# Kernel optimization log

Measured on AMD Instinct MI355X. Metric: run time of the kernel, lower is better.

Reference implementation:

```python
import jax, jax.numpy as jnp
import numpy as np

# FP4 lookup table (E2M1-style values) exactly as in FP4Codec.FP4_TABLE
FP4_TABLE = jnp.array([0.0, 0.5, 1.0, 1.5, 2.0, 3.0, 4.0, 6.0,
                       0.0, -0.5, -1.0, -1.5, -2.0, -3.0, -4.0, -6.0],
                      dtype=jnp.float32)

M, K, N = 128, 4096, 16384


def setup_inputs() -> dict:
    key = jax.random.key(0)
    k1, k2, k3, k4 = jax.random.split(key, 4)
    x = jax.random.normal(k1, (M, K), dtype=jnp.float32)
    # packed bytes: each int holds two 4-bit FP4 indices (hi<<4 | lo)
    weight_fp4 = jax.random.randint(k2, (N, K // 2), 0, 256, dtype=jnp.int32)
    # positive per-output-channel scale (encode guarantees >= 1e-8)
    weight_scale = jax.random.uniform(k3, (N,), dtype=jnp.float32,
                                      minval=1e-3, maxval=2e-2)
    bias = jax.random.normal(k4, (N,), dtype=jnp.float32) * 0.02
    return {"x": x, "weight_fp4": weight_fp4,
            "weight_scale": weight_scale, "bias": bias}


def _dequantize(weight_fp4, weight_scale):
    p = weight_fp4.astype(jnp.uint8)
    hi = (p >> 4) & 0xF
    lo = p & 0xF
    # interleave [hi, lo] along last dim -> [N, K] indices
    idx = jnp.stack([hi, lo], axis=-1).reshape(p.shape[0], -1)
    return FP4_TABLE[idx] * weight_scale[:, None]  # [N, K] fp32


def reference(x, weight_fp4, weight_scale, bias):
    w = _dequantize(weight_fp4, weight_scale)          # [N, K]
    y = jnp.einsum('mk,nk->mn', x, w) + bias            # [M, N]
    return jax.nn.gelu(y, approximate=False)            # exact GELU like F.gelu
```

## Files before the change

kernel.cpp:

```cpp
#include <hip/hip_runtime.h>
#include <stdint.h>


#define M_DIM 128
#define K_DIM 4096
#define N_DIM 16384
#define BN    64
#define BK    64
#define NK    (K_DIM/BK)
#define NT    512
#define NBLK  (N_DIM/BN)

#define A_BYTES 16384
#define B_BYTES 8192
#define NBUF    4
#define AOFF(b) ((b)*A_BYTES)
#define BOFF(b) (NBUF*A_BYTES + (b)*B_BYTES)
#define LDS_SZ  (NBUF*(A_BYTES+B_BYTES))

typedef __attribute__((ext_vector_type(8))) __bf16 bf16x8;
typedef __attribute__((ext_vector_type(4))) float  f32x4;
typedef unsigned short ushort_t;

__device__ __forceinline__ unsigned f2b_bits(float f) {
  unsigned u = __builtin_bit_cast(unsigned, f);
  u += 0x7FFFu + ((u >> 16) & 1u);
  return u >> 16;
}

__global__ __launch_bounds__(256) void convert_x_kernel(
    const float* __restrict__ x, ushort_t* __restrict__ xb) {
  int i = (blockIdx.x * blockDim.x + threadIdx.x) * 4;
  float4 v = *(const float4*)(x + i);
  ushort4 p;
  p.x = (ushort_t)f2b_bits(v.x);
  p.y = (ushort_t)f2b_bits(v.y);
  p.z = (ushort_t)f2b_bits(v.z);
  p.w = (ushort_t)f2b_bits(v.w);
  *(ushort4*)(xb + i) = p;
}

__device__ __forceinline__ void gl16(const void* g, void* l) {
  __builtin_amdgcn_global_load_lds(
      (const __attribute__((address_space(1))) void*)g,
      (__attribute__((address_space(3))) void*)l, 16, 0, 0);
}

__device__ __forceinline__ bf16x8 decode8(uint4 p) {
  unsigned u01 = __builtin_amdgcn_perm(p.y, p.x, 0x04000400u);
  unsigned u23 = __builtin_amdgcn_perm(p.w, p.z, 0x04000400u);
  unsigned q   = __builtin_amdgcn_perm(u23, u01, 0x05040100u);
  unsigned e  = (q >> 4) & 0x0F0F0F0Fu;
  unsigned o  = q & 0x0F0F0F0Fu;
  unsigned em = e & 0x07070707u, om = o & 0x07070707u;
  unsigned elo = __builtin_amdgcn_perm(0xC0804000u, 0xC0800000u, em);
  unsigned ehi = __builtin_amdgcn_perm(0x40404040u, 0x3F3F3F00u, em);
  unsigned olo = __builtin_amdgcn_perm(0xC0804000u, 0xC0800000u, om);
  unsigned ohi = __builtin_amdgcn_perm(0x40404040u, 0x3F3F3F00u, om);
  ehi |= (e & 0x08080808u) << 4;
  ohi |= (o & 0x08080808u) << 4;
  unsigned t0 = __builtin_amdgcn_perm(ehi, elo, 0x05010400u);
  unsigned t1 = __builtin_amdgcn_perm(ohi, olo, 0x05010400u);
  unsigned t2 = __builtin_amdgcn_perm(ehi, elo, 0x07030602u);
  unsigned t3 = __builtin_amdgcn_perm(ohi, olo, 0x07030602u);
  uint4 r;
  r.x = __builtin_amdgcn_perm(t1, t0, 0x05040100u);
  r.y = __builtin_amdgcn_perm(t1, t0, 0x07060302u);
  r.z = __builtin_amdgcn_perm(t3, t2, 0x05040100u);
  r.w = __builtin_amdgcn_perm(t3, t2, 0x07060302u);
  return __builtin_bit_cast(bf16x8, r);
}

#define MFMA16(a_, b_, c_) __builtin_amdgcn_mfma_f32_16x16x32_bf16(a_, b_, c_, 0, 0, 0)

template<bool USE_XB>
__global__ __launch_bounds__(NT) void fp4gemm_kernel(
    const void* __restrict__ xsrc,
    const int*  __restrict__ wq,
    const float* __restrict__ scale,
    const float* __restrict__ bias,
    float* __restrict__ out) {
  __shared__ __align__(16) uint8_t lds[LDS_SZ];

  const int t   = threadIdx.x;
  const int w   = t >> 6;
  const int l   = t & 63;
  const int l16 = l & 15;
  const int lq  = l >> 4;
  const int kh  = w >> 2;
  const int mh  = (w >> 1) & 1;
  const int nh  = w & 1;

  const int bid = blockIdx.x;
  const int n0  = ((bid & 7) * (NBLK / 8) + (bid >> 3)) * BN;

  const int srow = t >> 3;
  const int scol = (t & 7) * 16;
  const int sswz = (srow & 7) << 4;
  const int scbs = scol ^ sswz;
  const int bwr  = srow * 128 + (scol ^ sswz);

  const uint8_t* xb  = (const uint8_t*)xsrc;
  const uint8_t* wqb = (const uint8_t*)wq;

  uint4 rq0, rq1, rq2, rq3;

#define ISSUE_A(k_, b_) do { \
  gl16(xb + (size_t)(srow) * 8192 + (size_t)(k_) * 128 + scbs, \
       lds + AOFF(b_) + w * 1024); \
  gl16(xb + (size_t)(64 + srow) * 8192 + (size_t)(k_) * 128 + scbs, \
       lds + AOFF(b_) + 8192 + w * 1024); \
} while (0)

#define ISSUE_B(k_, s_) do { \
  rq##s_ = *(const uint4*)(wqb + (size_t)(n0 + srow) * 8192 + \
                           (size_t)(k_) * 128 + scol); \
} while (0)

#define DECODE_B(s_, b_) do { \
  *(bf16x8*)(lds + BOFF(b_) + bwr) = decode8(rq##s_); \
} while (0)

#define WAITV(N_) asm volatile("s_waitcnt vmcnt(" #N_ ")" ::: "memory")
#define BARRIER() do { \
  asm volatile("s_waitcnt lgkmcnt(0)" ::: "memory"); \
  __builtin_amdgcn_s_barrier(); \
  __builtin_amdgcn_sched_barrier(0); \
} while (0)

  f32x4 acc[4][2] = {{{0,0,0,0},{0,0,0,0}},{{0,0,0,0},{0,0,0,0}},
                     {{0,0,0,0},{0,0,0,0}},{{0,0,0,0},{0,0,0,0}}};

  const int cS  = ((lq << 4) + (kh << 6)) ^ ((l16 & 7) << 4);
  const int aR0 = (mh * 64 + l16) * 128;
  const int bR0 = (nh * 32 + l16) * 128;

#define COMPUTE(b_) do { \
  const uint8_t* Ab_ = lds + AOFF(b_); \
  const uint8_t* Bb_ = lds + BOFF(b_); \
  bf16x8 bf0_ = *(const bf16x8*)(Bb_ + bR0 + cS); \
  bf16x8 bf1_ = *(const bf16x8*)(Bb_ + bR0 + 2048 + cS); \
  _Pragma("unroll") \
  for (int r_ = 0; r_ < 4; ++r_) { \
    bf16x8 af_ = *(const bf16x8*)(Ab_ + aR0 + r_ * 2048 + cS); \
    acc[r_][0] = MFMA16(af_, bf0_, acc[r_][0]); \
    acc[r_][1] = MFMA16(af_, bf1_, acc[r_][1]); \
  } \
} while (0)

#define BODY(k_, u_, ab_, cb_) do { \
  WAITV(6); \
  BARRIER(); \
  DECODE_B(u_, u_); \
  ISSUE_B((k_) + 6, u_); \
  ISSUE_A((k_) + 3, ab_); \
  COMPUTE(cb_); \
} while (0)

  if constexpr (USE_XB) {
    ISSUE_B(0, 0); ISSUE_B(1, 1); ISSUE_B(2, 2); ISSUE_B(3, 3);
    ISSUE_A(0, 0); ISSUE_A(1, 1); ISSUE_A(2, 2);
    WAITV(6);
    DECODE_B(0, 0); DECODE_B(1, 1);
    ISSUE_B(4, 0); ISSUE_B(5, 1);
    WAITV(6); BARRIER();
    DECODE_B(2, 2); ISSUE_B(6, 2); ISSUE_A(3, 3); COMPUTE(0);
    WAITV(6); BARRIER();
    DECODE_B(3, 3); ISSUE_B(7, 3); ISSUE_A(4, 0); COMPUTE(1);
    for (int j = 0; j < 14; ++j) {
      BODY(2 + 4 * j, 0, 1, 2);
      BODY(3 + 4 * j, 1, 2, 3);
      BODY(4 + 4 * j, 2, 3, 0);
      BODY(5 + 4 * j, 3, 0, 1);
    }
    WAITV(6); BARRIER(); DECODE_B(0, 0); ISSUE_A(61, 1); COMPUTE(2);
    WAITV(5); BARRIER(); DECODE_B(1, 1); ISSUE_A(62, 2); COMPUTE(3);
    WAITV(4); BARRIER(); DECODE_B(2, 2); ISSUE_A(63, 3); COMPUTE(0);
    WAITV(4); BARRIER(); DECODE_B(3, 3); COMPUTE(1);
    WAITV(2); BARRIER(); COMPUTE(2);
    WAITV(0); BARRIER(); COMPUTE(3);
  } else {
    for (int kt = 0; kt < NK; ++kt) {
      __syncthreads();
#pragma unroll
      for (int i = 0; i < 2; ++i) {
        const float* xf = (const float*)xsrc +
            (size_t)(i * 64 + srow) * K_DIM + (size_t)kt * BK + (scol >> 1);
        float4 v0 = *(const float4*)(xf);
        float4 v1 = *(const float4*)(xf + 4);
        uint4 pk = make_uint4(f2b_bits(v0.x) | (f2b_bits(v0.y) << 16),
                              f2b_bits(v0.z) | (f2b_bits(v0.w) << 16),
                              f2b_bits(v1.x) | (f2b_bits(v1.y) << 16),
                              f2b_bits(v1.z) | (f2b_bits(v1.w) << 16));
        *(uint4*)(lds + AOFF(kt & 1) + (size_t)(i * 64 + srow) * 128 +
                  (scol ^ sswz)) = pk;
      }
      {
        uint4 pv = *(const uint4*)(wqb + (size_t)(n0 + srow) * 8192 +
                                   (size_t)kt * 128 + scol);
        *(bf16x8*)(lds + BOFF(kt & 1) + bwr) = decode8(pv);
      }
      __syncthreads();
      COMPUTE(kt & 1);
    }
  }

  __syncthreads();
  {
    uint8_t* red = lds;
    const int pos = w & 3;
    if (w >= 4) {
#pragma unroll
      for (int r = 0; r < 4; ++r)
#pragma unroll
        for (int c = 0; c < 2; ++c)
          *(f32x4*)(red + pos * 8192 + (r * 2 + c) * 1024 + l * 16) = acc[r][c];
    }
    __syncthreads();
    if (w < 4) {
#pragma unroll
      for (int r = 0; r < 4; ++r)
#pragma unroll
        for (int c = 0; c < 2; ++c)
          acc[r][c] += *(const f32x4*)(red + pos * 8192 + (r * 2 + c) * 1024 + l * 16);

#pragma unroll
      for (int c = 0; c < 2; ++c) {
        const int ngc = n0 + nh * 32 + c * 16 + l16;
        const float s  = scale[ngc];
        const float bb = bias[ngc];
#pragma unroll
        for (int r = 0; r < 4; ++r) {
#pragma unroll
          for (int j = 0; j < 4; ++j) {
            int m = mh * 64 + r * 16 + lq * 4 + j;
            float y = acc[r][c][j] * s + bb;
            float g = 0.5f * y * (1.0f + erff(y * 0.70710678118654752f));
            out[(size_t)m * N_DIM + ngc] = g;
          }
        }
      }
    }
  }
#undef ISSUE_A
#undef ISSUE_B
#undef DECODE_B
#undef WAITV
#undef BARRIER
#undef COMPUTE
#undef BODY
}

extern "C" void kernel_launch(void* const* d_in, const int* in_sizes, int n_in,
                              void* d_out, int out_size, void* d_ws, size_t ws_size,
                              hipStream_t stream) {
  const float* x     = (const float*)d_in[0];
  const int*   wq    = (const int*)d_in[1];
  const float* scale = (const float*)d_in[2];
  const float* bias  = (const float*)d_in[3];
  float* out = (float*)d_out;

  const size_t xb_bytes = (size_t)M_DIM * K_DIM * 2;
  if (ws_size >= xb_bytes) {
    ushort_t* xb = (ushort_t*)d_ws;
    convert_x_kernel<<<(M_DIM * K_DIM) / (256 * 4), 256, 0, stream>>>(x, xb);
    fp4gemm_kernel<true><<<NBLK, NT, 0, stream>>>(xb, wq, scale, bias, out);
  } else {
    fp4gemm_kernel<false><<<NBLK, NT, 0, stream>>>(x, wq, scale, bias, out);
  }
}
```

Baseline: 41.78 us.

## Load MFMA operands straight from global into registers, dropping LDS staging

The main GEMM kernel no longer stages x and weight tiles through LDS with barriers. Each lane loads its own MFMA fragments directly from global memory into a four-deep register ring and decodes FP4 weights in registers before the MFMA. This removes LDS write/read traffic and per-step barriers, at the cost of more registers and possibly less coalesced or redundant global loads, since x rows are re-read by every wave. The fallback path is rewritten as a separate simpler kernel.

```diff
diff --git a/kernel.cpp b/kernel.cpp
--- a/kernel.cpp
+++ b/kernel.cpp
@@ -5,18 +5,8 @@
 #define M_DIM 128
 #define K_DIM 4096
 #define N_DIM 16384
-#define BN    64
-#define BK    64
-#define NK    (K_DIM/BK)
 #define NT    512
-#define NBLK  (N_DIM/BN)
-
-#define A_BYTES 16384
-#define B_BYTES 8192
-#define NBUF    4
-#define AOFF(b) ((b)*A_BYTES)
-#define BOFF(b) (NBUF*A_BYTES + (b)*B_BYTES)
-#define LDS_SZ  (NBUF*(A_BYTES+B_BYTES))
+#define NBLK  256
 
 typedef __attribute__((ext_vector_type(8))) __bf16 bf16x8;
 typedef __attribute__((ext_vector_type(4))) float  f32x4;
@@ -38,12 +28,6 @@
   p.z = (ushort_t)f2b_bits(v.z);
   p.w = (ushort_t)f2b_bits(v.w);
   *(ushort4*)(xb + i) = p;
-}
-
-__device__ __forceinline__ void gl16(const void* g, void* l) {
-  __builtin_amdgcn_global_load_lds(
-      (const __attribute__((address_space(1))) void*)g,
-      (__attribute__((address_space(3))) void*)l, 16, 0, 0);
 }
 
 __device__ __forceinline__ bf16x8 decode8(uint4 p) {
@@ -73,14 +57,13 @@
 
 #define MFMA16(a_, b_, c_) __builtin_amdgcn_mfma_f32_16x16x32_bf16(a_, b_, c_, 0, 0, 0)
 
-template<bool USE_XB>
-__global__ __launch_bounds__(NT) void fp4gemm_kernel(
-    const void* __restrict__ xsrc,
+__global__ __launch_bounds__(NT) void fp4gemm_direct_kernel(
+    const ushort_t* __restrict__ xsrc,
     const int*  __restrict__ wq,
     const float* __restrict__ scale,
     const float* __restrict__ bias,
     float* __restrict__ out) {
-  __shared__ __align__(16) uint8_t lds[LDS_SZ];
+  __shared__ __align__(16) uint8_t lds[32768];
 
   const int t   = threadIdx.x;
   const int w   = t >> 6;
@@ -92,118 +75,47 @@
   const int nh  = w & 1;
 
   const int bid = blockIdx.x;
-  const int n0  = ((bid & 7) * (NBLK / 8) + (bid >> 3)) * BN;
-
-  const int srow = t >> 3;
-  const int scol = (t & 7) * 16;
-  const int sswz = (srow & 7) << 4;
-  const int scbs = scol ^ sswz;
-  const int bwr  = srow * 128 + (scol ^ sswz);
-
-  const uint8_t* xb  = (const uint8_t*)xsrc;
-  const uint8_t* wqb = (const uint8_t*)wq;
-
-  uint4 rq0, rq1, rq2, rq3;
-
-#define ISSUE_A(k_, b_) do { \
-  gl16(xb + (size_t)(srow) * 8192 + (size_t)(k_) * 128 + scbs, \
-       lds + AOFF(b_) + w * 1024); \
-  gl16(xb + (size_t)(64 + srow) * 8192 + (size_t)(k_) * 128 + scbs, \
-       lds + AOFF(b_) + 8192 + w * 1024); \
-} while (0)
-
-#define ISSUE_B(k_, s_) do { \
-  rq##s_ = *(const uint4*)(wqb + (size_t)(n0 + srow) * 8192 + \
-                           (size_t)(k_) * 128 + scol); \
-} while (0)
-
-#define DECODE_B(s_, b_) do { \
-  *(bf16x8*)(lds + BOFF(b_) + bwr) = decode8(rq##s_); \
-} while (0)
-
-#define WAITV(N_) asm volatile("s_waitcnt vmcnt(" #N_ ")" ::: "memory")
-#define BARRIER() do { \
-  asm volatile("s_waitcnt lgkmcnt(0)" ::: "memory"); \
-  __builtin_amdgcn_s_barrier(); \
-  __builtin_amdgcn_sched_barrier(0); \
-} while (0)
+  const int n0  = ((bid & 7) * 32 + (bid >> 3)) * 64;
+
+  const uint8_t* aB = (const uint8_t*)xsrc +
+      (size_t)(mh * 64 + l16) * 8192 + kh * 64 + lq * 16;
+  const uint8_t* bB = (const uint8_t*)wq +
+      (size_t)(n0 + nh * 32 + l16) * 8192 + kh * 64 + lq * 16;
 
   f32x4 acc[4][2] = {{{0,0,0,0},{0,0,0,0}},{{0,0,0,0},{0,0,0,0}},
                      {{0,0,0,0},{0,0,0,0}},{{0,0,0,0},{0,0,0,0}}};
 
-  const int cS  = ((lq << 4) + (kh << 6)) ^ ((l16 & 7) << 4);
-  const int aR0 = (mh * 64 + l16) * 128;
-  const int bR0 = (nh * 32 + l16) * 128;
-
-#define COMPUTE(b_) do { \
-  const uint8_t* Ab_ = lds + AOFF(b_); \
-  const uint8_t* Bb_ = lds + BOFF(b_); \
-  bf16x8 bf0_ = *(const bf16x8*)(Bb_ + bR0 + cS); \
-  bf16x8 bf1_ = *(const bf16x8*)(Bb_ + bR0 + 2048 + cS); \
+  uint4 sa0[4], sa1[4], sa2[4], sa3[4];
+  uint4 sb0[2], sb1[2], sb2[2], sb3[2];
+
+#define LOAD(kt_, s_) do { \
+  _Pragma("unroll") \
+  for (int r_ = 0; r_ < 4; ++r_) \
+    sa##s_[r_] = *(const uint4*)(aB + (size_t)r_ * 131072 + (kt_) * 128); \
+  _Pragma("unroll") \
+  for (int c_ = 0; c_ < 2; ++c_) \
+    sb##s_[c_] = *(const uint4*)(bB + (size_t)c_ * 131072 + (kt_) * 128); \
+} while (0)
+
+#define COMP(s_) do { \
+  bf16x8 pb0_ = decode8(sb##s_[0]); \
+  bf16x8 pb1_ = decode8(sb##s_[1]); \
   _Pragma("unroll") \
   for (int r_ = 0; r_ < 4; ++r_) { \
-    bf16x8 af_ = *(const bf16x8*)(Ab_ + aR0 + r_ * 2048 + cS); \
-    acc[r_][0] = MFMA16(af_, bf0_, acc[r_][0]); \
-    acc[r_][1] = MFMA16(af_, bf1_, acc[r_][1]); \
+    bf16x8 ar_ = __builtin_bit_cast(bf16x8, sa##s_[r_]); \
+    acc[r_][0] = MFMA16(ar_, pb0_, acc[r_][0]); \
+    acc[r_][1] = MFMA16(ar_, pb1_, acc[r_][1]); \
   } \
 } while (0)
 
-#define BODY(k_, u_, ab_, cb_) do { \
-  WAITV(6); \
-  BARRIER(); \
-  DECODE_B(u_, u_); \
-  ISSUE_B((k_) + 6, u_); \
-  ISSUE_A((k_) + 3, ab_); \
-  COMPUTE(cb_); \
-} while (0)
-
-  if constexpr (USE_XB) {
-    ISSUE_B(0, 0); ISSUE_B(1, 1); ISSUE_B(2, 2); ISSUE_B(3, 3);
-    ISSUE_A(0, 0); ISSUE_A(1, 1); ISSUE_A(2, 2);
-    WAITV(6);
-    DECODE_B(0, 0); DECODE_B(1, 1);
-    ISSUE_B(4, 0); ISSUE_B(5, 1);
-    WAITV(6); BARRIER();
-    DECODE_B(2, 2); ISSUE_B(6, 2); ISSUE_A(3, 3); COMPUTE(0);
-    WAITV(6); BARRIER();
-    DECODE_B(3, 3); ISSUE_B(7, 3); ISSUE_A(4, 0); COMPUTE(1);
-    for (int j = 0; j < 14; ++j) {
-      BODY(2 + 4 * j, 0, 1, 2);
-      BODY(3 + 4 * j, 1, 2, 3);
-      BODY(4 + 4 * j, 2, 3, 0);
-      BODY(5 + 4 * j, 3, 0, 1);
-    }
-    WAITV(6); BARRIER(); DECODE_B(0, 0); ISSUE_A(61, 1); COMPUTE(2);
-    WAITV(5); BARRIER(); DECODE_B(1, 1); ISSUE_A(62, 2); COMPUTE(3);
-    WAITV(4); BARRIER(); DECODE_B(2, 2); ISSUE_A(63, 3); COMPUTE(0);
-    WAITV(4); BARRIER(); DECODE_B(3, 3); COMPUTE(1);
-    WAITV(2); BARRIER(); COMPUTE(2);
-    WAITV(0); BARRIER(); COMPUTE(3);
-  } else {
-    for (int kt = 0; kt < NK; ++kt) {
-      __syncthreads();
-#pragma unroll
-      for (int i = 0; i < 2; ++i) {
-        const float* xf = (const float*)xsrc +
-            (size_t)(i * 64 + srow) * K_DIM + (size_t)kt * BK + (scol >> 1);
-        float4 v0 = *(const float4*)(xf);
-        float4 v1 = *(const float4*)(xf + 4);
-        uint4 pk = make_uint4(f2b_bits(v0.x) | (f2b_bits(v0.y) << 16),
-                              f2b_bits(v0.z) | (f2b_bits(v0.w) << 16),
-                              f2b_bits(v1.x) | (f2b_bits(v1.y) << 16),
-                              f2b_bits(v1.z) | (f2b_bits(v1.w) << 16));
-        *(uint4*)(lds + AOFF(kt & 1) + (size_t)(i * 64 + srow) * 128 +
-                  (scol ^ sswz)) = pk;
-      }
-      {
-        uint4 pv = *(const uint4*)(wqb + (size_t)(n0 + srow) * 8192 +
-                                   (size_t)kt * 128 + scol);
-        *(bf16x8*)(lds + BOFF(kt & 1) + bwr) = decode8(pv);
-      }
-      __syncthreads();
-      COMPUTE(kt & 1);
-    }
-  }
+  LOAD(0, 0); LOAD(1, 1); LOAD(2, 2); LOAD(3, 3);
+  for (int kt = 0; kt < 60; kt += 4) {
+    COMP(0); LOAD(kt + 4, 0);
+    COMP(1); LOAD(kt + 5, 1);
+    COMP(2); LOAD(kt + 6, 2);
+    COMP(3); LOAD(kt + 7, 3);
+  }
+  COMP(0); COMP(1); COMP(2); COMP(3);
 
   __syncthreads();
   {
@@ -242,13 +154,81 @@
       }
     }
   }
-#undef ISSUE_A
-#undef ISSUE_B
-#undef DECODE_B
-#undef WAITV
-#undef BARRIER
-#undef COMPUTE
-#undef BODY
+#undef LOAD
+#undef COMP
+}
+
+__global__ __launch_bounds__(NT) void fp4gemm_fallback_kernel(
+    const float* __restrict__ x, const int* __restrict__ wq,
+    const float* __restrict__ scale, const float* __restrict__ bias,
+    float* __restrict__ out) {
+  __shared__ __align__(16) uint8_t lds[49152];
+  const int t = threadIdx.x, w = t >> 6, l = t & 63;
+  const int l16 = l & 15, lq = l >> 4, mq = w >> 1, nh = w & 1;
+  const int n0 = (int)blockIdx.x * 64;
+  const int srow = t >> 3, scol = (t & 7) * 16, sswz = (srow & 7) << 4;
+  const int bwr = srow * 128 + (scol ^ sswz);
+  const uint8_t* wqb = (const uint8_t*)wq;
+  f32x4 acc00 = {0,0,0,0}, acc01 = {0,0,0,0};
+  f32x4 acc10 = {0,0,0,0}, acc11 = {0,0,0,0};
+  const int aR0 = (mq * 32 + l16) * 128;
+  const int bR0 = (nh * 32 + l16) * 128;
+  const int cB  = (lq << 4) ^ ((l16 & 7) << 4);
+  for (int kt = 0; kt < 64; ++kt) {
+    __syncthreads();
+    int bb = kt & 1;
+#pragma unroll
+    for (int i = 0; i < 2; ++i) {
+      const float* xf = x + (size_t)(i * 64 + srow) * K_DIM + (size_t)kt * 64 + (scol >> 1);
+      float4 v0 = *(const float4*)(xf);
+      float4 v1 = *(const float4*)(xf + 4);
+      uint4 pk = make_uint4(f2b_bits(v0.x) | (f2b_bits(v0.y) << 16),
+                            f2b_bits(v0.z) | (f2b_bits(v0.w) << 16),
+                            f2b_bits(v1.x) | (f2b_bits(v1.y) << 16),
+                            f2b_bits(v1.z) | (f2b_bits(v1.w) << 16));
+      *(uint4*)(lds + bb * 16384 + (size_t)(i * 64 + srow) * 128 + (scol ^ sswz)) = pk;
+    }
+    {
+      uint4 pv = *(const uint4*)(wqb + (size_t)(n0 + srow) * 8192 + (size_t)kt * 128 + scol);
+      *(bf16x8*)(lds + 32768 + bb * 8192 + bwr) = decode8(pv);
+    }
+    __syncthreads();
+    {
+      const uint8_t* Ab_ = lds + bb * 16384;
+      const uint8_t* Bb_ = lds + 32768 + bb * 8192;
+#pragma unroll
+      for (int ks = 0; ks < 2; ++ks) {
+        const int cS = (ks << 6) ^ cB;
+        bf16x8 a0 = *(const bf16x8*)(Ab_ + aR0 + cS);
+        bf16x8 a1 = *(const bf16x8*)(Ab_ + aR0 + 2048 + cS);
+        bf16x8 b0 = *(const bf16x8*)(Bb_ + bR0 + cS);
+        bf16x8 b1 = *(const bf16x8*)(Bb_ + bR0 + 2048 + cS);
+        acc00 = MFMA16(a0, b0, acc00);
+        acc01 = MFMA16(a0, b1, acc01);
+        acc10 = MFMA16(a1, b0, acc10);
+        acc11 = MFMA16(a1, b1, acc11);
+      }
+    }
+  }
+#pragma unroll
+  for (int c = 0; c < 2; ++c) {
+    const int ngc = n0 + nh * 32 + c * 16 + l16;
+    const float s = scale[ngc];
+    const float bv = bias[ngc];
+    f32x4 v0 = c ? acc01 : acc00;
+    f32x4 v1 = c ? acc11 : acc10;
+#pragma unroll
+    for (int fr = 0; fr < 2; ++fr) {
+      f32x4 vv = fr ? v1 : v0;
+#pragma unroll
+      for (int j = 0; j < 4; ++j) {
+        int m = mq * 32 + fr * 16 + lq * 4 + j;
+        float y = vv[j] * s + bv;
+        out[(size_t)m * N_DIM + ngc] =
+            0.5f * y * (1.0f + erff(y * 0.70710678118654752f));
+      }
+    }
+  }
 }
 
 extern "C" void kernel_launch(void* const* d_in, const int* in_sizes, int n_in,
@@ -264,8 +244,9 @@
   if (ws_size >= xb_bytes) {
     ushort_t* xb = (ushort_t*)d_ws;
     convert_x_kernel<<<(M_DIM * K_DIM) / (256 * 4), 256, 0, stream>>>(x, xb);
-    fp4gemm_kernel<true><<<NBLK, NT, 0, stream>>>(xb, wq, scale, bias, out);
+    fp4gemm_direct_kernel<<<NBLK, NT, 0, stream>>>(xb, wq, scale, bias, out);
   } else {
-    fp4gemm_kernel<false><<<NBLK, NT, 0, stream>>>(x, wq, scale, bias, out);
-  }
-}
+    fp4gemm_fallback_kernel<<<N_DIM / 64, NT, 0, stream>>>(
+        x, wq, scale, bias, out);
+  }
+}
```

Measured after the change: 102.1 us. 144% more time.
